# Kernel tuning notes

Hardware: AMD Instinct MI355X
Metric: run time of the kernel (lower is better)

The kernel has to match this reference:

```python
import jax, jax.numpy as jnp
import numpy as np

N_NODES = 50000
N_EDGES = 800000


def setup_inputs() -> dict:
    key = jax.random.key(0)
    ks = jax.random.split(key, 8)
    x = jax.random.normal(ks[0], (N_NODES, 128), dtype=jnp.float32)
    edge_index = jax.random.randint(ks[1], (2, N_EDGES), 0, N_NODES, dtype=jnp.int64)
    # GCNConv weights (PyG: x @ W then propagate, bias after aggregation)
    W1 = jax.random.normal(ks[2], (128, 256), dtype=jnp.float32) / np.sqrt(128)
    b1 = jnp.zeros((256,), dtype=jnp.float32)
    W2 = jax.random.normal(ks[3], (256, 128), dtype=jnp.float32) / np.sqrt(256)
    b2 = jnp.zeros((128,), dtype=jnp.float32)
    # projection head
    fcW1 = jax.random.normal(ks[4], (128, 128), dtype=jnp.float32) / np.sqrt(128)
    fcb1 = jnp.zeros((128,), dtype=jnp.float32)
    fcW2 = jax.random.normal(ks[5], (128, 128), dtype=jnp.float32) / np.sqrt(128)
    fcb2 = jnp.zeros((128,), dtype=jnp.float32)
    return {"x": x, "edge_index": edge_index, "W1": W1, "b1": b1,
            "W2": W2, "b2": b2, "fcW1": fcW1, "fcb1": fcb1,
            "fcW2": fcW2, "fcb2": fcb2}


def _gcn_conv(x, W, b, src, dst, dinv):
    # x' = D^-1/2 (A + I) D^-1/2 (x W) + b  (GCN with self-loops)
    xw = x @ W                                             # [N, C]
    coeff = dinv[src] * dinv[dst]                          # [E]
    msg = xw[src] * coeff[:, None]                         # [E, C] gather
    agg = jax.ops.segment_sum(msg, dst, num_segments=N_NODES)  # scatter-add
    self_term = xw * (dinv * dinv)[:, None]                # self-loop
    return agg + self_term + b


def reference(x, edge_index, W1, b1, W2, b2, fcW1, fcb1, fcW2, fcb2):
    src, dst = edge_index[0], edge_index[1]
    # degree of A + I (in-degree on dst, weight 1 each, +1 self-loop)
    deg = jax.ops.segment_sum(jnp.ones((N_EDGES,), jnp.float32), dst,
                              num_segments=N_NODES) + 1.0
    dinv = jax.lax.rsqrt(deg)
    # Encoder: GCNConv -> relu -> GCNConv -> relu
    h = jax.nn.relu(_gcn_conv(x, W1, b1, src, dst, dinv))
    z = jax.nn.relu(_gcn_conv(h, W2, b2, src, dst, dinv))
    # projection: Linear -> ELU -> Linear
    p = jax.nn.elu(z @ fcW1 + fcb1)
    return p @ fcW2 + fcb2
```

## Files before the change

### kernel.cpp

```cpp
#include <hip/hip_runtime.h>
#include <hip/hip_bf16.h>
#include <cstdint>

#define N_NODES 50000
#define N_EDGES 800000
#define C128 128
#define SCAN_BLOCKS ((N_NODES + 255) / 256)

typedef __attribute__((ext_vector_type(8))) short bf16x8;
typedef __attribute__((ext_vector_type(4))) float f32x4;
typedef unsigned int u32;

__device__ __forceinline__ bf16x8 pack_bf16x8(u32 a, u32 b, u32 c, u32 d) {
    union { u32 u[4]; bf16x8 v; } x;
    x.u[0] = a; x.u[1] = b; x.u[2] = c; x.u[3] = d;
    return x.v;
}

__device__ __forceinline__ bf16x8 as_bf16x8(uint4 v) {
    union { uint4 u; bf16x8 b; } x;
    x.u = v;
    return x.b;
}

__device__ __forceinline__ u32 rne_bf16(float x) {
    u32 u = __float_as_uint(x);
    return (u + 0x7FFFu + ((u >> 16) & 1u)) >> 16;
}

__device__ __forceinline__ void stage16(const u32* g, u32* lds) {
    __builtin_amdgcn_global_load_lds(
        (const __attribute__((address_space(1))) u32*)g,
        (__attribute__((address_space(3))) u32*)lds, 16, 0, 0);
}


__global__ void k_zero(int* __restrict__ a, int* __restrict__ b, int n) {
    int i = blockIdx.x * blockDim.x + threadIdx.x;
    if (i < n) { a[i] = 0; b[i] = 0; }
}

__device__ __forceinline__ int clamp_node(int v) {
    return v < 0 ? 0 : (v >= N_NODES ? N_NODES - 1 : v);
}

__global__ void k_count(const int* __restrict__ ei, int* __restrict__ counts) {
    int e = blockIdx.x * blockDim.x + threadIdx.x;
    if (e < N_EDGES) {
        int dst = clamp_node(ei[N_EDGES + e]);
        atomicAdd(&counts[dst], 1);
    }
}

__global__ void k_dinv(const int* __restrict__ counts, float* __restrict__ dinv) {
    int i = blockIdx.x * blockDim.x + threadIdx.x;
    if (i < N_NODES) {
        dinv[i] = rsqrtf((float)counts[i] + 1.0f);
    }
}

__global__ __launch_bounds__(256) void k_xscale(const float* __restrict__ x,
                                                const float* __restrict__ dinv,
                                                u32* __restrict__ xs ) {
    int idx = blockIdx.x * 256 + threadIdx.x;
    if (idx < N_NODES * 32) {
        int node = idx >> 5;
        float di = dinv[node];
        float4 v = reinterpret_cast<const float4*>(x)[idx];
        u32 w0 = rne_bf16(v.x * di) | (rne_bf16(v.y * di) << 16);
        u32 w1 = rne_bf16(v.z * di) | (rne_bf16(v.w * di) << 16);
        reinterpret_cast<uint2*>(xs)[idx] = make_uint2(w0, w1);
    }
}

__global__ __launch_bounds__(256) void k_scan1(const int* __restrict__ counts,
                                               int* __restrict__ part,
                                               int* __restrict__ bsum) {
    __shared__ int s[256];
    const int tid = threadIdx.x;
    const int i = blockIdx.x * 256 + tid;
    int v = (i < N_NODES) ? counts[i] : 0;
    s[tid] = v;
    __syncthreads();
    for (int off = 1; off < 256; off <<= 1) {
        int t = (tid >= off) ? s[tid - off] : 0;
        __syncthreads();
        s[tid] += t;
        __syncthreads();
    }
    if (i < N_NODES) part[i] = s[tid];
    if (tid == 255) bsum[blockIdx.x] = s[255];
}

__global__ __launch_bounds__(256) void k_scan2(const int* __restrict__ bsum,
                                               int* __restrict__ boff) {
    __shared__ int s[256];
    const int tid = threadIdx.x;
    int v = (tid < SCAN_BLOCKS) ? bsum[tid] : 0;
    s[tid] = v;
    __syncthreads();
    for (int off = 1; off < 256; off <<= 1) {
        int t = (tid >= off) ? s[tid - off] : 0;
        __syncthreads();
        s[tid] += t;
        __syncthreads();
    }
    if (tid < SCAN_BLOCKS) boff[tid] = s[tid] - v;
}

__global__ __launch_bounds__(256) void k_scan3(const int* __restrict__ part,
                                               const int* __restrict__ counts,
                                               const int* __restrict__ boff,
                                               int* __restrict__ offsets) {
    const int i = blockIdx.x * 256 + threadIdx.x;
    if (i < N_NODES) offsets[i] = part[i] - counts[i] + boff[blockIdx.x];
    if (i == 0) offsets[N_NODES] = N_EDGES;
}

__global__ void k_fill(const int* __restrict__ ei, const int* __restrict__ offsets,
                       int* __restrict__ cursor, int* __restrict__ csr) {
    int e = blockIdx.x * blockDim.x + threadIdx.x;
    if (e < N_EDGES) {
        int src = clamp_node(ei[e]);
        int dst = clamp_node(ei[N_EDGES + e]);
        int pos = atomicAdd(&cursor[dst], 1);
        int slot = offsets[dst] + pos;
        if (slot < N_EDGES) csr[slot] = src;
    }
}


__global__ __launch_bounds__(64) void k_prep(const float* __restrict__ W1,
                                             const float* __restrict__ W2,
                                             const float* __restrict__ fcW1,
                                             const float* __restrict__ fcW2,
                                             u32* __restrict__ ftab) {
    int bx = blockIdx.x;
    int s = bx >> 5, f = bx & 31;
    int kf = f >> 3, nf = f & 7;
    int l = threadIdx.x;
    const float* src; int ld, roff, coff;
    switch (s) {
        case 0:  src = W1;   ld = 256; roff = 0;   coff = 0;   break;
        case 1:  src = W1;   ld = 256; roff = 0;   coff = 128; break;
        case 2:  src = W2;   ld = 128; roff = 0;   coff = 0;   break;
        case 3:  src = W2;   ld = 128; roff = 128; coff = 0;   break;
        case 4:  src = fcW1; ld = 128; roff = 0;   coff = 0;   break;
        default: src = fcW2; ld = 128; roff = 0;   coff = 0;   break;
    }
    int col = coff + nf * 16 + (l & 15);
    int krow = roff + kf * 32 + (l >> 4) * 8;
    u32 hp[4], lp[4];
#pragma unroll
    for (int p = 0; p < 4; ++p) {
        float a0 = src[(size_t)(krow + 2 * p) * ld + col];
        float a1 = src[(size_t)(krow + 2 * p + 1) * ld + col];
        u32 h0 = __float_as_uint(a0) & 0xFFFF0000u;
        u32 h1 = __float_as_uint(a1) & 0xFFFF0000u;
        float r0 = a0 - __uint_as_float(h0);
        float r1 = a1 - __uint_as_float(h1);
        hp[p] = (h0 >> 16) | h1;
        lp[p] = ((__float_as_uint(r0) & 0xFFFF0000u) >> 16) |
                (__float_as_uint(r1) & 0xFFFF0000u);
    }
    u32* dst = ftab + (size_t)bx * 512;
    *reinterpret_cast<uint4*>(dst + 4 * l)       = make_uint4(hp[0], hp[1], hp[2], hp[3]);
    *reinterpret_cast<uint4*>(dst + 256 + 4 * l) = make_uint4(lp[0], lp[1], lp[2], lp[3]);
}


template <bool HAS_BIAS, bool RELU>
__global__ __launch_bounds__(256) void k_prop(const u32* __restrict__ xs,
                                              float* __restrict__ out,
                                              const float* __restrict__ dinv,
                                              const int* __restrict__ offsets,
                                              const int* __restrict__ csr,
                                              const float* __restrict__ bias) {
    const int wave = threadIdx.x >> 6;
    const int lane = threadIdx.x & 63;
    const int half = lane >> 5;
    const int lc   = lane & 31;
    const int node = (blockIdx.x * 4 + wave) * 2 + half;
    if (node >= N_NODES) return;

    const uint2* __restrict__ xp = reinterpret_cast<const uint2*>(xs);
    const float di = dinv[node];

    uint2 sv = xp[(size_t)node * 32 + lc];
    float ax = __uint_as_float(sv.x << 16);
    float ay = __uint_as_float(sv.x & 0xFFFF0000u);
    float az = __uint_as_float(sv.y << 16);
    float aw = __uint_as_float(sv.y & 0xFFFF0000u);

    int e = offsets[node];
    const int eend = offsets[node + 1];
    for (; e + 4 <= eend; e += 4) {
        int s0 = csr[e + 0], s1 = csr[e + 1], s2 = csr[e + 2], s3 = csr[e + 3];
        uint2 v0 = xp[(size_t)s0 * 32 + lc];
        uint2 v1 = xp[(size_t)s1 * 32 + lc];
        uint2 v2 = xp[(size_t)s2 * 32 + lc];
        uint2 v3 = xp[(size_t)s3 * 32 + lc];
        ax += __uint_as_float(v0.x << 16);
        ay += __uint_as_float(v0.x & 0xFFFF0000u);
        az += __uint_as_float(v0.y << 16);
        aw += __uint_as_float(v0.y & 0xFFFF0000u);
        ax += __uint_as_float(v1.x << 16);
        ay += __uint_as_float(v1.x & 0xFFFF0000u);
        az += __uint_as_float(v1.y << 16);
        aw += __uint_as_float(v1.y & 0xFFFF0000u);
        ax += __uint_as_float(v2.x << 16);
        ay += __uint_as_float(v2.x & 0xFFFF0000u);
        az += __uint_as_float(v2.y << 16);
        aw += __uint_as_float(v2.y & 0xFFFF0000u);
        ax += __uint_as_float(v3.x << 16);
        ay += __uint_as_float(v3.x & 0xFFFF0000u);
        az += __uint_as_float(v3.y << 16);
        aw += __uint_as_float(v3.y & 0xFFFF0000u);
    }
    for (; e < eend; ++e) {
        int s = csr[e];
        uint2 v = xp[(size_t)s * 32 + lc];
        ax += __uint_as_float(v.x << 16);
        ay += __uint_as_float(v.x & 0xFFFF0000u);
        az += __uint_as_float(v.y << 16);
        aw += __uint_as_float(v.y & 0xFFFF0000u);
    }

    float4 o;
    o.x = di * ax; o.y = di * ay; o.z = di * az; o.w = di * aw;
    if (HAS_BIAS) {
        float4 bb = reinterpret_cast<const float4*>(bias)[lc];
        o.x += bb.x; o.y += bb.y; o.z += bb.z; o.w += bb.w;
    }
    if (RELU) {
        o.x = fmaxf(o.x, 0.0f); o.y = fmaxf(o.y, 0.0f);
        o.z = fmaxf(o.z, 0.0f); o.w = fmaxf(o.w, 0.0f);
    }
    reinterpret_cast<float4*>(out)[(size_t)node * 32 + lc] = o;
}


template <int NHALF, int ACT1, bool FINAL_BIAS, bool BF16_OUT>
__global__ __launch_bounds__(256) void k_fused(
        const float* __restrict__ A,
        const u32* __restrict__ ftabW1,
        const u32* __restrict__ ftabW2,
        const float* __restrict__ b1v,
        const float* __restrict__ b2v,
        float* __restrict__ C,
        u32* __restrict__ C16,
        const float* __restrict__ dscale,
        int M) {
    __shared__ u32 lds_w[2][4096];

    const int tid = threadIdx.x;
    const int wave = tid >> 6, l = tid & 63;
    const int l15 = l & 15, l4 = l >> 4;
    const int r = blockIdx.x * 64 + wave * 16 + l15;
    const float* arow = A + (size_t)(r < M ? r : M - 1) * 128;

    const int NSTEP = NHALF * 8;

    auto stepbase = [&](int s) -> const u32* {
        int half = (NHALF == 2) ? (s >> 3) : 0;
        int phase = (s >> 2) & 1;
        int kf = s & 3;
        const u32* sec = phase ? ftabW2 : ftabW1;
        return sec + (size_t)half * 16384 + kf * 4096;
    };
    auto stage_batch = [&](int s, int buf) {
        const u32* g = stepbase(s) + wave * 1024 + 4 * l;
        u32* lb = &lds_w[buf][wave * 1024];
        stage16(g, lb);
        stage16(g + 256, lb + 256);
        stage16(g + 512, lb + 512);
        stage16(g + 768, lb + 768);
    };

    f32x4 accQ[8] = {};
    int buf = 0;

    stage_batch(0, 0);
    __syncthreads();

    for (int half = 0; half < NHALF; ++half) {
        f32x4 accH[8] = {};
#pragma unroll
        for (int kf = 0; kf < 4; ++kf) {
            int s = half * 8 + kf;
            if (s + 1 < NSTEP) stage_batch(s + 1, buf ^ 1);

            const float* ap = arow + kf * 32 + l4 * 8;
            float4 v0 = *reinterpret_cast<const float4*>(ap);
            float4 v1 = *reinterpret_cast<const float4*>(ap + 4);
            float av[8] = {v0.x, v0.y, v0.z, v0.w, v1.x, v1.y, v1.z, v1.w};
            u32 hp[4], lp[4];
#pragma unroll
            for (int p = 0; p < 4; ++p) {
                float a0 = av[2 * p], a1 = av[2 * p + 1];
                u32 h0 = __float_as_uint(a0) & 0xFFFF0000u;
                u32 h1 = __float_as_uint(a1) & 0xFFFF0000u;
                float q0 = a0 - __uint_as_float(h0);
                float q1 = a1 - __uint_as_float(h1);
                hp[p] = (h0 >> 16) | h1;
                lp[p] = ((__float_as_uint(q0) & 0xFFFF0000u) >> 16) |
                        (__float_as_uint(q1) & 0xFFFF0000u);
            }
            bf16x8 ahi = pack_bf16x8(hp[0], hp[1], hp[2], hp[3]);
            bf16x8 alo = pack_bf16x8(lp[0], lp[1], lp[2], lp[3]);

            const u32* lb = lds_w[buf];
#pragma unroll
            for (int nf = 0; nf < 8; ++nf) {
                const u32* fb = lb + nf * 512;
                bf16x8 whi = as_bf16x8(*reinterpret_cast<const uint4*>(fb + 4 * l));
                bf16x8 wlo = as_bf16x8(*reinterpret_cast<const uint4*>(fb + 256 + 4 * l));
                accH[nf] = __builtin_amdgcn_mfma_f32_16x16x32_bf16(whi, ahi, accH[nf], 0, 0, 0);
                accH[nf] = __builtin_amdgcn_mfma_f32_16x16x32_bf16(whi, alo, accH[nf], 0, 0, 0);
                accH[nf] = __builtin_amdgcn_mfma_f32_16x16x32_bf16(wlo, ahi, accH[nf], 0, 0, 0);
            }
            __syncthreads();
            buf ^= 1;
        }

        u32 hpk[8][4];
#pragma unroll
        for (int nf = 0; nf < 8; ++nf) {
            const float4 bb = *reinterpret_cast<const float4*>(
                b1v + half * 128 + nf * 16 + l4 * 4);
            const float bbv[4] = {bb.x, bb.y, bb.z, bb.w};
#pragma unroll
            for (int reg = 0; reg < 4; ++reg) {
                float v = accH[nf][reg] + bbv[reg];
                if (ACT1 == 1) v = fmaxf(v, 0.0f);
                else           v = v > 0.0f ? v : (expf(v) - 1.0f);
                u32 vh = __float_as_uint(v) & 0xFFFF0000u;
                float rr = v - __uint_as_float(vh);
                hpk[nf][reg] = (vh >> 16) | (__float_as_uint(rr) & 0xFFFF0000u);
            }
        }

#pragma unroll
        for (int kf = 0; kf < 4; ++kf) {
            int s = half * 8 + 4 + kf;
            if (s + 1 < NSTEP) stage_batch(s + 1, buf ^ 1);

            u32 got[8];
#pragma unroll
            for (int je = 0; je < 8; ++je) {
                int srcLane = ((l4 & 1) * 2 + (je >> 2)) * 16 + l15;
                u32 g0 = __shfl(hpk[2 * kf][je & 3], srcLane, 64);
                u32 g1 = __shfl(hpk[2 * kf + 1][je & 3], srcLane, 64);
                got[je] = (l4 & 2) ? g1 : g0;
            }
            u32 hh[4], gg[4];
#pragma unroll
            for (int p = 0; p < 4; ++p) {
                hh[p] = (got[2 * p] & 0xFFFFu) | (got[2 * p + 1] << 16);
                gg[p] = (got[2 * p] >> 16) | (got[2 * p + 1] & 0xFFFF0000u);
            }
            bf16x8 bh = pack_bf16x8(hh[0], hh[1], hh[2], hh[3]);
            bf16x8 bl = pack_bf16x8(gg[0], gg[1], gg[2], gg[3]);

            const u32* lb = lds_w[buf];
#pragma unroll
            for (int nf = 0; nf < 8; ++nf) {
                const u32* fb = lb + nf * 512;
                bf16x8 whi = as_bf16x8(*reinterpret_cast<const uint4*>(fb + 4 * l));
                bf16x8 wlo = as_bf16x8(*reinterpret_cast<const uint4*>(fb + 256 + 4 * l));
                accQ[nf] = __builtin_amdgcn_mfma_f32_16x16x32_bf16(whi, bh, accQ[nf], 0, 0, 0);
                accQ[nf] = __builtin_amdgcn_mfma_f32_16x16x32_bf16(whi, bl, accQ[nf], 0, 0, 0);
                accQ[nf] = __builtin_amdgcn_mfma_f32_16x16x32_bf16(wlo, bh, accQ[nf], 0, 0, 0);
            }
            __syncthreads();
            buf ^= 1;
        }
    }

    if (r < M) {
        if (BF16_OUT) {
            float sc = dscale[r];
#pragma unroll
            for (int nf = 0; nf < 8; ++nf) {
                u32 w0 = rne_bf16(accQ[nf][0] * sc) | (rne_bf16(accQ[nf][1] * sc) << 16);
                u32 w1 = rne_bf16(accQ[nf][2] * sc) | (rne_bf16(accQ[nf][3] * sc) << 16);
                reinterpret_cast<uint2*>(C16)[(size_t)r * 32 + nf * 4 + l4] =
                    make_uint2(w0, w1);
            }
        } else {
#pragma unroll
            for (int nf = 0; nf < 8; ++nf) {
                float4 v;
                v.x = accQ[nf][0]; v.y = accQ[nf][1];
                v.z = accQ[nf][2]; v.w = accQ[nf][3];
                if (FINAL_BIAS) {
                    const float4 bb = *reinterpret_cast<const float4*>(b2v + nf * 16 + l4 * 4);
                    v.x += bb.x; v.y += bb.y; v.z += bb.z; v.w += bb.w;
                }
                *reinterpret_cast<float4*>(C + (size_t)r * 128 + nf * 16 + l4 * 4) = v;
            }
        }
    }
}


extern "C" void kernel_launch(void* const* d_in, const int* in_sizes, int n_in,
                              void* d_out, int out_size, void* d_ws, size_t ws_size,
                              hipStream_t stream) {
    const float* x    = (const float*)d_in[0];
    const int*   ei   = (const int*)d_in[1];
    const float* W1   = (const float*)d_in[2];
    const float* b1   = (const float*)d_in[3];
    const float* W2   = (const float*)d_in[4];
    const float* b2   = (const float*)d_in[5];
    const float* fcW1 = (const float*)d_in[6];
    const float* fcb1 = (const float*)d_in[7];
    const float* fcW2 = (const float*)d_in[8];
    const float* fcb2 = (const float*)d_in[9];
    float* out        = (float*)d_out;

    char* ws = (char*)d_ws;
    size_t off = 0;
    auto alloc = [&](size_t bytes) {
        void* p = ws + off;
        off += (bytes + 255) & ~(size_t)255;
        return p;
    };
    int*   counts  = (int*)alloc(N_NODES * sizeof(int));
    int*   cursor  = (int*)alloc(N_NODES * sizeof(int));
    int*   part    = (int*)alloc(N_NODES * sizeof(int));
    int*   bsum    = (int*)alloc(SCAN_BLOCKS * sizeof(int));
    int*   boff    = (int*)alloc(SCAN_BLOCKS * sizeof(int));
    int*   offsets = (int*)alloc((N_NODES + 1) * sizeof(int));
    int*   csr     = (int*)alloc(N_EDGES * sizeof(int));
    float* dinv    = (float*)alloc(N_NODES * sizeof(float));
    u32*   ftab    = (u32*)alloc((size_t)192 * 512 * sizeof(u32));
    u32*   xs      = (u32*)alloc((size_t)N_NODES * 128 * 2);
    u32*   qs      = (u32*)alloc((size_t)N_NODES * 128 * 2);
    (void)ws_size; (void)n_in; (void)in_sizes; (void)out_size;

    const u32 SEC = 16384;

    k_zero<<<(N_NODES + 255) / 256, 256, 0, stream>>>(counts, cursor, N_NODES);
    k_prep<<<192, 64, 0, stream>>>(W1, W2, fcW1, fcW2, ftab);
    k_count<<<(N_EDGES + 255) / 256, 256, 0, stream>>>(ei, counts);
    k_dinv<<<(N_NODES + 255) / 256, 256, 0, stream>>>(counts, dinv);
    k_xscale<<<(N_NODES * 32 + 255) / 256, 256, 0, stream>>>(x, dinv, xs);
    k_scan1<<<SCAN_BLOCKS, 256, 0, stream>>>(counts, part, bsum);
    k_scan2<<<1, 256, 0, stream>>>(bsum, boff);
    k_scan3<<<SCAN_BLOCKS, 256, 0, stream>>>(part, counts, boff, offsets);
    k_fill<<<(N_EDGES + 255) / 256, 256, 0, stream>>>(ei, offsets, cursor, csr);

    const int prop_grid = (N_NODES + 7) / 8;
    const int gm = (N_NODES + 63) / 64;

    k_prop<false, false><<<prop_grid, 256, 0, stream>>>(xs, out, dinv, offsets, csr, nullptr);

    k_fused<2, 1, false, true><<<gm, 256, 0, stream>>>(out, ftab, ftab + 2 * SEC,
                                                       b1, nullptr, nullptr, qs, dinv, N_NODES);

    k_prop<true, true><<<prop_grid, 256, 0, stream>>>(qs, out, dinv, offsets, csr, b2);

    k_fused<1, 2, true, false><<<gm, 256, 0, stream>>>(out, ftab + 4 * SEC, ftab + 5 * SEC,
                                                       fcb1, fcb2, out, nullptr, nullptr, N_NODES);
}
```

Baseline: 240.0 us.

## Stage whole weight sections in LDS and process two row tiles per wave

The fused MLP kernel now stages an entire 64KB weight section into LDS at once instead of double-buffering 16KB chunks, and each wave handles 32 rows (two 16-row tiles), so every LDS weight fragment feeds twice as many MFMAs. Fewer barriers are needed per K-step and the grid is halved. The weight table layout in prep is remapped to match. In exchange the kernel uses more LDS and registers, with a launch-bounds hint of 2 blocks, and loses the overlap between weight staging and compute.

```diff
diff --git a/kernel.cpp b/kernel.cpp
--- a/kernel.cpp
+++ b/kernel.cpp
@@ -163,7 +163,7 @@
         lp[p] = ((__float_as_uint(r0) & 0xFFFF0000u) >> 16) |
                 (__float_as_uint(r1) & 0xFFFF0000u);
     }
-    u32* dst = ftab + (size_t)bx * 512;
+    u32* dst = ftab + ((size_t)(bx >> 5)) * 16384 + (size_t)(f) * 512;
     *reinterpret_cast<uint4*>(dst + 4 * l)       = make_uint4(hp[0], hp[1], hp[2], hp[3]);
     *reinterpret_cast<uint4*>(dst + 256 + 4 * l) = make_uint4(lp[0], lp[1], lp[2], lp[3]);
 }
@@ -241,7 +241,7 @@
 
 
 template <int NHALF, int ACT1, bool FINAL_BIAS, bool BF16_OUT>
-__global__ __launch_bounds__(256) void k_fused(
+__global__ __launch_bounds__(256, 2) void k_fused(
         const float* __restrict__ A,
         const u32* __restrict__ ftabW1,
         const u32* __restrict__ ftabW2,
@@ -251,139 +251,146 @@
         u32* __restrict__ C16,
         const float* __restrict__ dscale,
         int M) {
-    __shared__ u32 lds_w[2][4096];
+    __shared__ u32 lds_w[16384];
 
     const int tid = threadIdx.x;
     const int wave = tid >> 6, l = tid & 63;
     const int l15 = l & 15, l4 = l >> 4;
-    const int r = blockIdx.x * 64 + wave * 16 + l15;
-    const float* arow = A + (size_t)(r < M ? r : M - 1) * 128;
-
-    const int NSTEP = NHALF * 8;
-
-    auto stepbase = [&](int s) -> const u32* {
-        int half = (NHALF == 2) ? (s >> 3) : 0;
-        int phase = (s >> 2) & 1;
-        int kf = s & 3;
-        const u32* sec = phase ? ftabW2 : ftabW1;
-        return sec + (size_t)half * 16384 + kf * 4096;
+    const int m_base = blockIdx.x * 128 + wave * 32;
+    const int r0 = m_base + l15, r1 = m_base + 16 + l15;
+    const float* arow0 = A + (size_t)(r0 < M ? r0 : M - 1) * 128;
+    const float* arow1 = A + (size_t)(r1 < M ? r1 : M - 1) * 128;
+
+    auto stage_sec = [&](const u32* sec) {
+#pragma unroll
+        for (int i = 0; i < 16; ++i) {
+            int off = i * 1024 + wave * 256;
+            stage16(sec + off + 4 * l, lds_w + off);
+        }
     };
-    auto stage_batch = [&](int s, int buf) {
-        const u32* g = stepbase(s) + wave * 1024 + 4 * l;
-        u32* lb = &lds_w[buf][wave * 1024];
-        stage16(g, lb);
-        stage16(g + 256, lb + 256);
-        stage16(g + 512, lb + 512);
-        stage16(g + 768, lb + 768);
-    };
-
-    f32x4 accQ[8] = {};
-    int buf = 0;
-
-    stage_batch(0, 0);
+
+    f32x4 accQ[2][8] = {};
+
+    stage_sec(ftabW1);
     __syncthreads();
 
+#pragma unroll
     for (int half = 0; half < NHALF; ++half) {
-        f32x4 accH[8] = {};
+        f32x4 accH[2][8] = {};
 #pragma unroll
         for (int kf = 0; kf < 4; ++kf) {
-            int s = half * 8 + kf;
-            if (s + 1 < NSTEP) stage_batch(s + 1, buf ^ 1);
-
-            const float* ap = arow + kf * 32 + l4 * 8;
-            float4 v0 = *reinterpret_cast<const float4*>(ap);
-            float4 v1 = *reinterpret_cast<const float4*>(ap + 4);
-            float av[8] = {v0.x, v0.y, v0.z, v0.w, v1.x, v1.y, v1.z, v1.w};
-            u32 hp[4], lp[4];
-#pragma unroll
-            for (int p = 0; p < 4; ++p) {
-                float a0 = av[2 * p], a1 = av[2 * p + 1];
-                u32 h0 = __float_as_uint(a0) & 0xFFFF0000u;
-                u32 h1 = __float_as_uint(a1) & 0xFFFF0000u;
-                float q0 = a0 - __uint_as_float(h0);
-                float q1 = a1 - __uint_as_float(h1);
-                hp[p] = (h0 >> 16) | h1;
-                lp[p] = ((__float_as_uint(q0) & 0xFFFF0000u) >> 16) |
-                        (__float_as_uint(q1) & 0xFFFF0000u);
-            }
-            bf16x8 ahi = pack_bf16x8(hp[0], hp[1], hp[2], hp[3]);
-            bf16x8 alo = pack_bf16x8(lp[0], lp[1], lp[2], lp[3]);
-
-            const u32* lb = lds_w[buf];
+            bf16x8 ahi[2], alo[2];
+#pragma unroll
+            for (int t = 0; t < 2; ++t) {
+                const float* ap = (t == 0 ? arow0 : arow1) + kf * 32 + l4 * 8;
+                float4 v0 = *reinterpret_cast<const float4*>(ap);
+                float4 v1 = *reinterpret_cast<const float4*>(ap + 4);
+                float av[8] = {v0.x, v0.y, v0.z, v0.w, v1.x, v1.y, v1.z, v1.w};
+                u32 hp[4], lp[4];
+#pragma unroll
+                for (int p = 0; p < 4; ++p) {
+                    float a0 = av[2 * p], a1 = av[2 * p + 1];
+                    u32 h0 = __float_as_uint(a0) & 0xFFFF0000u;
+                    u32 h1 = __float_as_uint(a1) & 0xFFFF0000u;
+                    float q0 = a0 - __uint_as_float(h0);
+                    float q1 = a1 - __uint_as_float(h1);
+                    hp[p] = (h0 >> 16) | h1;
+                    lp[p] = ((__float_as_uint(q0) & 0xFFFF0000u) >> 16) |
+                            (__float_as_uint(q1) & 0xFFFF0000u);
+                }
+                ahi[t] = pack_bf16x8(hp[0], hp[1], hp[2], hp[3]);
+                alo[t] = pack_bf16x8(lp[0], lp[1], lp[2], lp[3]);
+            }
 #pragma unroll
             for (int nf = 0; nf < 8; ++nf) {
-                const u32* fb = lb + nf * 512;
+                const u32* fb = lds_w + (kf * 8 + nf) * 512;
                 bf16x8 whi = as_bf16x8(*reinterpret_cast<const uint4*>(fb + 4 * l));
                 bf16x8 wlo = as_bf16x8(*reinterpret_cast<const uint4*>(fb + 256 + 4 * l));
-                accH[nf] = __builtin_amdgcn_mfma_f32_16x16x32_bf16(whi, ahi, accH[nf], 0, 0, 0);
-                accH[nf] = __builtin_amdgcn_mfma_f32_16x16x32_bf16(whi, alo, accH[nf], 0, 0, 0);
-                accH[nf] = __builtin_amdgcn_mfma_f32_16x16x32_bf16(wlo, ahi, accH[nf], 0, 0, 0);
-            }
-            __syncthreads();
-            buf ^= 1;
-        }
-
-        u32 hpk[8][4];
+#pragma unroll
+                for (int t = 0; t < 2; ++t) {
+                    accH[t][nf] = __builtin_amdgcn_mfma_f32_16x16x32_bf16(whi, ahi[t], accH[t][nf], 0, 0, 0);
+                    accH[t][nf] = __builtin_amdgcn_mfma_f32_16x16x32_bf16(whi, alo[t], accH[t][nf], 0, 0, 0);
+                    accH[t][nf] = __builtin_amdgcn_mfma_f32_16x16x32_bf16(wlo, ahi[t], accH[t][nf], 0, 0, 0);
+                }
+            }
+        }
+        __syncthreads();
+        stage_sec(ftabW2 + (size_t)half * 16384);
+
+        u32 hpk[2][8][4];
 #pragma unroll
         for (int nf = 0; nf < 8; ++nf) {
             const float4 bb = *reinterpret_cast<const float4*>(
                 b1v + half * 128 + nf * 16 + l4 * 4);
             const float bbv[4] = {bb.x, bb.y, bb.z, bb.w};
 #pragma unroll
-            for (int reg = 0; reg < 4; ++reg) {
-                float v = accH[nf][reg] + bbv[reg];
-                if (ACT1 == 1) v = fmaxf(v, 0.0f);
-                else           v = v > 0.0f ? v : (expf(v) - 1.0f);
-                u32 vh = __float_as_uint(v) & 0xFFFF0000u;
-                float rr = v - __uint_as_float(vh);
-                hpk[nf][reg] = (vh >> 16) | (__float_as_uint(rr) & 0xFFFF0000u);
-            }
-        }
+            for (int t = 0; t < 2; ++t) {
+#pragma unroll
+                for (int reg = 0; reg < 4; ++reg) {
+                    float v = accH[t][nf][reg] + bbv[reg];
+                    if (ACT1 == 1) v = fmaxf(v, 0.0f);
+                    else           v = v > 0.0f ? v : (expf(v) - 1.0f);
+                    u32 vh = __float_as_uint(v) & 0xFFFF0000u;
+                    float rr = v - __uint_as_float(vh);
+                    hpk[t][nf][reg] = (vh >> 16) | (__float_as_uint(rr) & 0xFFFF0000u);
+                }
+            }
+        }
+        __syncthreads();
 
 #pragma unroll
         for (int kf = 0; kf < 4; ++kf) {
-            int s = half * 8 + 4 + kf;
-            if (s + 1 < NSTEP) stage_batch(s + 1, buf ^ 1);
-
-            u32 got[8];
-#pragma unroll
-            for (int je = 0; je < 8; ++je) {
-                int srcLane = ((l4 & 1) * 2 + (je >> 2)) * 16 + l15;
-                u32 g0 = __shfl(hpk[2 * kf][je & 3], srcLane, 64);
-                u32 g1 = __shfl(hpk[2 * kf + 1][je & 3], srcLane, 64);
-                got[je] = (l4 & 2) ? g1 : g0;
-            }
-            u32 hh[4], gg[4];
-#pragma unroll
-            for (int p = 0; p < 4; ++p) {
-                hh[p] = (got[2 * p] & 0xFFFFu) | (got[2 * p + 1] << 16);
-                gg[p] = (got[2 * p] >> 16) | (got[2 * p + 1] & 0xFFFF0000u);
-            }
-            bf16x8 bh = pack_bf16x8(hh[0], hh[1], hh[2], hh[3]);
-            bf16x8 bl = pack_bf16x8(gg[0], gg[1], gg[2], gg[3]);
-
-            const u32* lb = lds_w[buf];
+            bf16x8 bh[2], bl[2];
+#pragma unroll
+            for (int t = 0; t < 2; ++t) {
+                u32 got[8];
+#pragma unroll
+                for (int je = 0; je < 8; ++je) {
+                    int srcLane = ((l4 & 1) * 2 + (je >> 2)) * 16 + l15;
+                    u32 g0 = __shfl(hpk[t][2 * kf][je & 3], srcLane, 64);
+                    u32 g1 = __shfl(hpk[t][2 * kf + 1][je & 3], srcLane, 64);
+                    got[je] = (l4 & 2) ? g1 : g0;
+                }
+                u32 hh[4], gg[4];
+#pragma unroll
+                for (int p = 0; p < 4; ++p) {
+                    hh[p] = (got[2 * p] & 0xFFFFu) | (got[2 * p + 1] << 16);
+                    gg[p] = (got[2 * p] >> 16) | (got[2 * p + 1] & 0xFFFF0000u);
+                }
+                bh[t] = pack_bf16x8(hh[0], hh[1], hh[2], hh[3]);
+                bl[t] = pack_bf16x8(gg[0], gg[1], gg[2], gg[3]);
+            }
 #pragma unroll
             for (int nf = 0; nf < 8; ++nf) {
-                const u32* fb = lb + nf * 512;
+                const u32* fb = lds_w + (kf * 8 + nf) * 512;
                 bf16x8 whi = as_bf16x8(*reinterpret_cast<const uint4*>(fb + 4 * l));
                 bf16x8 wlo = as_bf16x8(*reinterpret_cast<const uint4*>(fb + 256 + 4 * l));
-                accQ[nf] = __builtin_amdgcn_mfma_f32_16x16x32_bf16(whi, bh, accQ[nf], 0, 0, 0);
-                accQ[nf] = __builtin_amdgcn_mfma_f32_16x16x32_bf16(whi, bl, accQ[nf], 0, 0, 0);
-                accQ[nf] = __builtin_amdgcn_mfma_f32_16x16x32_bf16(wlo, bh, accQ[nf], 0, 0, 0);
-            }
+#pragma unroll
+                for (int t = 0; t < 2; ++t) {
+                    accQ[t][nf] = __builtin_amdgcn_mfma_f32_16x16x32_bf16(whi, bh[t], accQ[t][nf], 0, 0, 0);
+                    accQ[t][nf] = __builtin_amdgcn_mfma_f32_16x16x32_bf16(whi, bl[t], accQ[t][nf], 0, 0, 0);
+                    accQ[t][nf] = __builtin_amdgcn_mfma_f32_16x16x32_bf16(wlo, bh[t], accQ[t][nf], 0, 0, 0);
+                }
+            }
+        }
+
+        if (half + 1 < NHALF) {
             __syncthreads();
-            buf ^= 1;
-        }
-    }
-
-    if (r < M) {
+            stage_sec(ftabW1 + (size_t)(half + 1) * 16384);
+            __syncthreads();
+        }
+    }
+
+#pragma unroll
+    for (int t = 0; t < 2; ++t) {
+        int r = (t == 0) ? r0 : r1;
+        if (r >= M) continue;
         if (BF16_OUT) {
             float sc = dscale[r];
 #pragma unroll
             for (int nf = 0; nf < 8; ++nf) {
-                u32 w0 = rne_bf16(accQ[nf][0] * sc) | (rne_bf16(accQ[nf][1] * sc) << 16);
-                u32 w1 = rne_bf16(accQ[nf][2] * sc) | (rne_bf16(accQ[nf][3] * sc) << 16);
+                u32 w0 = rne_bf16(accQ[t][nf][0] * sc) | (rne_bf16(accQ[t][nf][1] * sc) << 16);
+                u32 w1 = rne_bf16(accQ[t][nf][2] * sc) | (rne_bf16(accQ[t][nf][3] * sc) << 16);
                 reinterpret_cast<uint2*>(C16)[(size_t)r * 32 + nf * 4 + l4] =
                     make_uint2(w0, w1);
             }
@@ -391,8 +398,8 @@
 #pragma unroll
             for (int nf = 0; nf < 8; ++nf) {
                 float4 v;
-                v.x = accQ[nf][0]; v.y = accQ[nf][1];
-                v.z = accQ[nf][2]; v.w = accQ[nf][3];
+                v.x = accQ[t][nf][0]; v.y = accQ[t][nf][1];
+                v.z = accQ[t][nf][2]; v.w = accQ[t][nf][3];
                 if (FINAL_BIAS) {
                     const float4 bb = *reinterpret_cast<const float4*>(b2v + nf * 16 + l4 * 4);
                     v.x += bb.x; v.y += bb.y; v.z += bb.z; v.w += bb.w;
@@ -434,7 +441,7 @@
     int*   offsets = (int*)alloc((N_NODES + 1) * sizeof(int));
     int*   csr     = (int*)alloc(N_EDGES * sizeof(int));
     float* dinv    = (float*)alloc(N_NODES * sizeof(float));
-    u32*   ftab    = (u32*)alloc((size_t)192 * 512 * sizeof(u32));
+    u32*   ftab    = (u32*)alloc((size_t)6 * 16384 * sizeof(u32));
     u32*   xs      = (u32*)alloc((size_t)N_NODES * 128 * 2);
     u32*   qs      = (u32*)alloc((size_t)N_NODES * 128 * 2);
     (void)ws_size; (void)n_in; (void)in_sizes; (void)out_size;
@@ -452,7 +459,7 @@
     k_fill<<<(N_EDGES + 255) / 256, 256, 0, stream>>>(ei, offsets, cursor, csr);
 
     const int prop_grid = (N_NODES + 7) / 8;
-    const int gm = (N_NODES + 63) / 64;
+    const int gm = (N_NODES + 127) / 128;
 
     k_prop<false, false><<<prop_grid, 256, 0, stream>>>(xs, out, dinv, offsets, csr, nullptr);
 
```

Measured after the change: 226.7 us. -5.5%, faster.

## Keep hi weight section resident in LDS, stream lo weights from global

Applied to the files above, without the earlier changes.

The weight table is re-laid out so each 128x128 section stores all hi-bf16 fragments contiguously, followed by all lo fragments. The fused GEMM kernel stages a whole hi section into LDS once per phase and loads lo fragments straight from global/L2 into registers. This replaces per-k-step double-buffered staging and its barrier after every k-step. A launch-bounds occupancy hint of 3 is added. The trade-off is more global loads and more register pressure for the lo weights, plus exposed staging latency between phases.

```diff
diff --git a/kernel.cpp b/kernel.cpp
--- a/kernel.cpp
+++ b/kernel.cpp
@@ -163,9 +163,9 @@
         lp[p] = ((__float_as_uint(r0) & 0xFFFF0000u) >> 16) |
                 (__float_as_uint(r1) & 0xFFFF0000u);
     }
-    u32* dst = ftab + (size_t)bx * 512;
-    *reinterpret_cast<uint4*>(dst + 4 * l)       = make_uint4(hp[0], hp[1], hp[2], hp[3]);
-    *reinterpret_cast<uint4*>(dst + 256 + 4 * l) = make_uint4(lp[0], lp[1], lp[2], lp[3]);
+    u32* secb = ftab + (size_t)s * 16384;
+    *reinterpret_cast<uint4*>(secb + (size_t)f * 256 + 4 * l)        = make_uint4(hp[0], hp[1], hp[2], hp[3]);
+    *reinterpret_cast<uint4*>(secb + 8192 + (size_t)f * 256 + 4 * l) = make_uint4(lp[0], lp[1], lp[2], lp[3]);
 }
 
 
@@ -241,7 +241,7 @@
 
 
 template <int NHALF, int ACT1, bool FINAL_BIAS, bool BF16_OUT>
-__global__ __launch_bounds__(256) void k_fused(
+__global__ __launch_bounds__(256, 3) void k_fused(
         const float* __restrict__ A,
         const u32* __restrict__ ftabW1,
         const u32* __restrict__ ftabW2,
@@ -251,7 +251,7 @@
         u32* __restrict__ C16,
         const float* __restrict__ dscale,
         int M) {
-    __shared__ u32 lds_w[2][4096];
+    __shared__ u32 lds_w[8192];
 
     const int tid = threadIdx.x;
     const int wave = tid >> 6, l = tid & 63;
@@ -259,36 +259,32 @@
     const int r = blockIdx.x * 64 + wave * 16 + l15;
     const float* arow = A + (size_t)(r < M ? r : M - 1) * 128;
 
-    const int NSTEP = NHALF * 8;
-
-    auto stepbase = [&](int s) -> const u32* {
-        int half = (NHALF == 2) ? (s >> 3) : 0;
-        int phase = (s >> 2) & 1;
-        int kf = s & 3;
-        const u32* sec = phase ? ftabW2 : ftabW1;
-        return sec + (size_t)half * 16384 + kf * 4096;
+    auto stage_hi = [&](const u32* sec) {
+#pragma unroll
+        for (int i = 0; i < 8; ++i) {
+            int off = i * 1024 + wave * 256;
+            stage16(sec + off + 4 * l, lds_w + off);
+        }
     };
-    auto stage_batch = [&](int s, int buf) {
-        const u32* g = stepbase(s) + wave * 1024 + 4 * l;
-        u32* lb = &lds_w[buf][wave * 1024];
-        stage16(g, lb);
-        stage16(g + 256, lb + 256);
-        stage16(g + 512, lb + 512);
-        stage16(g + 768, lb + 768);
-    };
 
     f32x4 accQ[8] = {};
-    int buf = 0;
-
-    stage_batch(0, 0);
+
+    stage_hi(ftabW1);
     __syncthreads();
 
+#pragma unroll
     for (int half = 0; half < NHALF; ++half) {
+        const u32* w1lo = ftabW1 + (size_t)half * 16384 + 8192;
+        const u32* w2lo = ftabW2 + (size_t)half * 16384 + 8192;
+
         f32x4 accH[8] = {};
 #pragma unroll
         for (int kf = 0; kf < 4; ++kf) {
-            int s = half * 8 + kf;
-            if (s + 1 < NSTEP) stage_batch(s + 1, buf ^ 1);
+            uint4 wl[8];
+#pragma unroll
+            for (int nf = 0; nf < 8; ++nf)
+                wl[nf] = *reinterpret_cast<const uint4*>(
+                    w1lo + (size_t)(kf * 8 + nf) * 256 + 4 * l);
 
             const float* ap = arow + kf * 32 + l4 * 8;
             float4 v0 = *reinterpret_cast<const float4*>(ap);
@@ -309,19 +305,18 @@
             bf16x8 ahi = pack_bf16x8(hp[0], hp[1], hp[2], hp[3]);
             bf16x8 alo = pack_bf16x8(lp[0], lp[1], lp[2], lp[3]);
 
-            const u32* lb = lds_w[buf];
 #pragma unroll
             for (int nf = 0; nf < 8; ++nf) {
-                const u32* fb = lb + nf * 512;
-                bf16x8 whi = as_bf16x8(*reinterpret_cast<const uint4*>(fb + 4 * l));
-                bf16x8 wlo = as_bf16x8(*reinterpret_cast<const uint4*>(fb + 256 + 4 * l));
+                bf16x8 whi = as_bf16x8(*reinterpret_cast<const uint4*>(
+                    lds_w + (kf * 8 + nf) * 256 + 4 * l));
+                bf16x8 wlo = as_bf16x8(wl[nf]);
                 accH[nf] = __builtin_amdgcn_mfma_f32_16x16x32_bf16(whi, ahi, accH[nf], 0, 0, 0);
                 accH[nf] = __builtin_amdgcn_mfma_f32_16x16x32_bf16(whi, alo, accH[nf], 0, 0, 0);
                 accH[nf] = __builtin_amdgcn_mfma_f32_16x16x32_bf16(wlo, ahi, accH[nf], 0, 0, 0);
             }
-            __syncthreads();
-            buf ^= 1;
-        }
+        }
+        __syncthreads();
+        stage_hi(ftabW2 + (size_t)half * 16384);
 
         u32 hpk[8][4];
 #pragma unroll
@@ -339,11 +334,15 @@
                 hpk[nf][reg] = (vh >> 16) | (__float_as_uint(rr) & 0xFFFF0000u);
             }
         }
+        __syncthreads();
 
 #pragma unroll
         for (int kf = 0; kf < 4; ++kf) {
-            int s = half * 8 + 4 + kf;
-            if (s + 1 < NSTEP) stage_batch(s + 1, buf ^ 1);
+            uint4 wl[8];
+#pragma unroll
+            for (int nf = 0; nf < 8; ++nf)
+                wl[nf] = *reinterpret_cast<const uint4*>(
+                    w2lo + (size_t)(kf * 8 + nf) * 256 + 4 * l);
 
             u32 got[8];
 #pragma unroll
@@ -362,18 +361,21 @@
             bf16x8 bh = pack_bf16x8(hh[0], hh[1], hh[2], hh[3]);
             bf16x8 bl = pack_bf16x8(gg[0], gg[1], gg[2], gg[3]);
 
-            const u32* lb = lds_w[buf];
 #pragma unroll
             for (int nf = 0; nf < 8; ++nf) {
-                const u32* fb = lb + nf * 512;
-                bf16x8 whi = as_bf16x8(*reinterpret_cast<const uint4*>(fb + 4 * l));
-                bf16x8 wlo = as_bf16x8(*reinterpret_cast<const uint4*>(fb + 256 + 4 * l));
+                bf16x8 whi = as_bf16x8(*reinterpret_cast<const uint4*>(
+                    lds_w + (kf * 8 + nf) * 256 + 4 * l));
+                bf16x8 wlo = as_bf16x8(wl[nf]);
                 accQ[nf] = __builtin_amdgcn_mfma_f32_16x16x32_bf16(whi, bh, accQ[nf], 0, 0, 0);
                 accQ[nf] = __builtin_amdgcn_mfma_f32_16x16x32_bf16(whi, bl, accQ[nf], 0, 0, 0);
                 accQ[nf] = __builtin_amdgcn_mfma_f32_16x16x32_bf16(wlo, bh, accQ[nf], 0, 0, 0);
             }
+        }
+
+        if (half + 1 < NHALF) {
             __syncthreads();
-            buf ^= 1;
+            stage_hi(ftabW1 + (size_t)(half + 1) * 16384);
+            __syncthreads();
         }
     }
 
@@ -434,7 +436,7 @@
     int*   offsets = (int*)alloc((N_NODES + 1) * sizeof(int));
     int*   csr     = (int*)alloc(N_EDGES * sizeof(int));
     float* dinv    = (float*)alloc(N_NODES * sizeof(float));
-    u32*   ftab    = (u32*)alloc((size_t)192 * 512 * sizeof(u32));
+    u32*   ftab    = (u32*)alloc((size_t)6 * 16384 * sizeof(u32));
     u32*   xs      = (u32*)alloc((size_t)N_NODES * 128 * 2);
     u32*   qs      = (u32*)alloc((size_t)N_NODES * 128 * 2);
     (void)ws_size; (void)n_in; (void)in_sizes; (void)out_size;
```

After: 238.6 us. About the same (-0.6%).
